# Kernel tuning notes

Hardware: AMD Instinct MI355X
Metric: run time of the kernel (lower is better)

Reference implementation:

```python
import jax, jax.numpy as jnp
import numpy as np

B, S, I, H, O = 64, 2048, 256, 512, 10

def setup_inputs() -> dict:
    key = jax.random.key(0)
    ks = jax.random.split(key, 16)
    s_in = 1.0 / np.sqrt(I)
    s_h = 1.0 / np.sqrt(H)
    return {
        "x": jax.random.normal(ks[0], (B, S, I), dtype=jnp.float32),
        "Wz": jax.random.normal(ks[1], (H, I), dtype=jnp.float32) * s_in,
        "bz": jax.random.normal(ks[2], (H,), dtype=jnp.float32) * s_in,
        "Uz": jax.random.normal(ks[3], (H, H), dtype=jnp.float32) * s_h,
        "cz": jax.random.normal(ks[4], (H,), dtype=jnp.float32) * s_h,
        "Wr": jax.random.normal(ks[5], (H, I), dtype=jnp.float32) * s_in,
        "br": jax.random.normal(ks[6], (H,), dtype=jnp.float32) * s_in,
        "Ur": jax.random.normal(ks[7], (H, H), dtype=jnp.float32) * s_h,
        "cr": jax.random.normal(ks[8], (H,), dtype=jnp.float32) * s_h,
        "Wh": jax.random.normal(ks[9], (H, I), dtype=jnp.float32) * s_in,
        "bh": jax.random.normal(ks[10], (H,), dtype=jnp.float32) * s_in,
        "Uh": jax.random.normal(ks[11], (H, H), dtype=jnp.float32) * s_h,
        "ch": jax.random.normal(ks[12], (H,), dtype=jnp.float32) * s_h,
        "Wf": jax.random.normal(ks[13], (O, H), dtype=jnp.float32) * s_h,
        "bf": jax.random.normal(ks[14], (O,), dtype=jnp.float32) * s_h,
    }


def reference(x, Wz, bz, Uz, cz, Wr, br, Ur, cr, Wh, bh, Uh, ch, Wf, bf):
    b, s, _ = x.shape
    h_dim = Uz.shape[0]
    # Precompute input-gate projections for all timesteps in 3 big GEMMs: [B,S,H]
    xz = jnp.einsum('bsi,hi->bsh', x, Wz) + bz
    xr = jnp.einsum('bsi,hi->bsh', x, Wr) + br
    xh = jnp.einsum('bsi,hi->bsh', x, Wh) + bh
    # scan over time (transpose to time-major [S,B,H])
    xs = (jnp.swapaxes(xz, 0, 1), jnp.swapaxes(xr, 0, 1), jnp.swapaxes(xh, 0, 1))

    def step(h, ins):
        xz_t, xr_t, xh_t = ins
        z = jax.nn.sigmoid(xz_t + h @ Uz.T + cz)
        r = jax.nn.sigmoid(xr_t + h @ Ur.T + cr)
        h_tilde = jnp.tanh(xh_t + (r * h) @ Uh.T + ch)
        h_new = (1.0 - z) * h + z * h_tilde
        return h_new, None

    h0 = jnp.zeros((b, h_dim), dtype=x.dtype)
    h_T, _ = jax.lax.scan(step, h0, xs)
    return h_T @ Wf.T + bf
```

## Files before the change

kernel.cpp:

```cpp
#include <hip/hip_runtime.h>
#include <stdint.h>


#define S_LEN  2048
#define BATCH  64
#define IDIM   256
#define HDIM   512
#define ODIM   10
#define GATES3 1536

typedef __attribute__((ext_vector_type(8))) short bf16x8;
typedef __attribute__((ext_vector_type(4))) float f32x4;

__device__ __forceinline__ unsigned short f2bf(float x) {
    unsigned int u = __float_as_uint(x);
    u += 0x7fffu + ((u >> 16) & 1u);
    return (unsigned short)(u >> 16);
}
__device__ __forceinline__ float bf2f(unsigned short h) {
    return __uint_as_float(((unsigned int)h) << 16);
}

__device__ __forceinline__ unsigned long long g_load64(const void* p) {
    return __hip_atomic_load((const unsigned long long*)p, __ATOMIC_RELAXED, __HIP_MEMORY_SCOPE_AGENT);
}
__device__ __forceinline__ void g_store32(void* p, unsigned int v) {
    __hip_atomic_store((unsigned int*)p, v, __ATOMIC_RELAXED, __HIP_MEMORY_SCOPE_AGENT);
}

__global__ __launch_bounds__(256)
void proj_mfma(const float* __restrict__ x,
               const float* __restrict__ Wz, const float* __restrict__ Wr, const float* __restrict__ Wh,
               const float* __restrict__ bz, const float* __restrict__ cz,
               const float* __restrict__ br, const float* __restrict__ cr,
               const float* __restrict__ bh, const float* __restrict__ ch,
               unsigned short* __restrict__ xp2)
{
    __shared__ unsigned short As[8 * 128 * 8];
    __shared__ unsigned short Bs[8 * 128 * 8];
    const int tid  = threadIdx.x;
    const int wave = tid >> 6;
    const int lane = tid & 63;
    const int quad = lane >> 4;
    const int l16  = lane & 15;
    const int nt_ = blockIdx.x;
    const int mt_ = blockIdx.y;

    const int srow  = tid >> 1;
    const int shalf = tid & 1;
    const int mg = mt_ * 128 + srow;
    const float* axrow = x + ((size_t)(mg & 63) * S_LEN + (mg >> 6)) * IDIM + shalf * 32;
    const int ng = nt_ * 128 + srow;
    const int gt = ng >> 9, hl = ng & 511;
    const float* bxrow = (gt == 0 ? Wz : gt == 1 ? Wr : Wh) + (size_t)hl * IDIM + shalf * 32;

    f32x4 acc[2][8];
#pragma unroll
    for (int mi = 0; mi < 2; ++mi)
#pragma unroll
        for (int nj = 0; nj < 8; ++nj) {
            f32x4 z = {0.f, 0.f, 0.f, 0.f};
            acc[mi][nj] = z;
        }

    for (int kp = 0; kp < IDIM; kp += 64) {
#pragma unroll
        for (int c = 0; c < 4; ++c) {
            unsigned short ta[8], tb[8];
#pragma unroll
            for (int e = 0; e < 8; ++e) {
                ta[e] = f2bf(axrow[kp + c * 8 + e]);
                tb[e] = f2bf(bxrow[kp + c * 8 + e]);
            }
            const int kcq = shalf * 4 + c;
            *(bf16x8*)(As + (kcq * 128 + srow) * 8) = *(bf16x8*)ta;
            *(bf16x8*)(Bs + (kcq * 128 + srow) * 8) = *(bf16x8*)tb;
        }
        __syncthreads();
#pragma unroll
        for (int kc = 0; kc < 2; ++kc) {
            bf16x8 af[2], bfr[8];
#pragma unroll
            for (int mi = 0; mi < 2; ++mi)
                af[mi] = *(const bf16x8*)(As + ((kc * 4 + quad) * 128 + wave * 32 + mi * 16 + l16) * 8);
#pragma unroll
            for (int nj = 0; nj < 8; ++nj)
                bfr[nj] = *(const bf16x8*)(Bs + ((kc * 4 + quad) * 128 + nj * 16 + l16) * 8);
#pragma unroll
            for (int mi = 0; mi < 2; ++mi)
#pragma unroll
                for (int nj = 0; nj < 8; ++nj)
                    acc[mi][nj] = __builtin_amdgcn_mfma_f32_16x16x32_bf16(af[mi], bfr[nj], acc[mi][nj], 0, 0, 0);
        }
        __syncthreads();
    }

    const int s_ = mt_ * 2 + (wave >> 1);
#pragma unroll
    for (int nj = 0; nj < 8; ++nj) {
        const int n  = nt_ * 128 + nj * 16 + l16;
        const int g2 = n >> 9, h2 = n & 511;
        const float bias = (g2 == 0 ? bz[h2] + cz[h2]
                          : g2 == 1 ? br[h2] + cr[h2]
                                    : bh[h2] + ch[h2]);
#pragma unroll
        for (int mi = 0; mi < 2; ++mi) {
            const int gg = (wave & 1) * 2 + mi;
            unsigned short pk[4];
#pragma unroll
            for (int r = 0; r < 4; ++r) pk[r] = f2bf(acc[mi][nj][r] + bias);
            *(unsigned long long*)(xp2 + (((size_t)gg * S_LEN + s_) * GATES3 + n) * 16 + quad * 4) =
                *(unsigned long long*)pk;
        }
    }
}

__device__ __forceinline__ void stage_frag(const unsigned short* __restrict__ gsrc,
                                           unsigned short* __restrict__ lds, int tid)
{
    unsigned long long v[8];
    const unsigned short* p = gsrc + tid * 32;
#pragma unroll
    for (int i = 0; i < 8; ++i) v[i] = g_load64(p + i * 4);
    unsigned long long* q = (unsigned long long*)(lds + tid * 32);
#pragma unroll
    for (int i = 0; i < 8; ++i) q[i] = v[i];
}

__device__ __forceinline__ void group_barrier(unsigned int* __restrict__ flags, int g, int j,
                                              unsigned int epoch, int tid, int lane)
{
    __syncthreads();
    if (tid == 0)
        __hip_atomic_store(&flags[(g * 16 + j) * 16], epoch,
                           __ATOMIC_RELAXED, __HIP_MEMORY_SCOPE_AGENT);
    if (lane < 16) {
        const unsigned int* f = &flags[(g * 16 + lane) * 16];
        while (__hip_atomic_load(f, __ATOMIC_RELAXED, __HIP_MEMORY_SCOPE_AGENT) < epoch)
            __builtin_amdgcn_s_sleep(2);
    }
}

__global__ __launch_bounds__(256)
void gru_recur(const float* __restrict__ Uz, const float* __restrict__ Ur,
               const float* __restrict__ Uh,
               const unsigned short* __restrict__ xp2,
               unsigned short* __restrict__ hg,
               unsigned short* __restrict__ rhg,
               float* __restrict__ hgf,
               unsigned int* __restrict__ flags,
               const float* __restrict__ Wf, const float* __restrict__ bfv,
               float* __restrict__ out)
{
    __shared__ unsigned short ldsA[8192];
    __shared__ unsigned short ldsB[8192];
    __shared__ float hlds[16][33];
    const int tid  = threadIdx.x;
    const int wave = tid >> 6;
    const int lane = tid & 63;
    const int quad = lane >> 4;
    const int l16  = lane & 15;
    const int g  = blockIdx.x & 3;
    const int j  = blockIdx.x >> 2;
    const int b0 = g * 16;
    const int i0 = j * 32;
    const int nt = wave & 1;
    const bool isZ = (wave < 2);

    for (int i = tid; i < 16 * 33; i += 256) (&hlds[0][0])[i] = 0.f;

    const int wrow = i0 + nt * 16 + l16;
    const int kofs = quad * 8;
    bf16x8 wp1[16], wp2[16];
    const float* U1 = isZ ? Uz : Ur;
#pragma unroll
    for (int kb = 0; kb < 16; ++kb) {
        const float* s1 = U1 + (size_t)wrow * HDIM + kb * 32 + kofs;
        const float* s2 = Uh + (size_t)wrow * HDIM + kb * 32 + kofs;
        bf16x8 w1, w2;
#pragma unroll
        for (int e = 0; e < 8; ++e) {
            w1[e] = (short)f2bf(s1[e]);
            w2[e] = (short)f2bf(s2[e]);
        }
        wp1[kb] = w1; wp2[kb] = w2;
    }

    const int iloc = nt * 16 + l16;
    const int icol = i0 + iloc;
    const int pidx = (icol >> 5) * 512 + ((icol >> 3) & 3) * 128 + (icol & 7);
    unsigned short* hgG  = hg  + g * 8192;
    unsigned short* rhgG = rhg + g * 8192;
    const unsigned short* xpg = xp2 + (size_t)g * S_LEN * GATES3 * 16;
    const int gofs1 = isZ ? 0 : HDIM;

    float zfrag[4];
    float hm[4] = {0.f, 0.f, 0.f, 0.f};

    unsigned long long xg_cur = *(const unsigned long long*)
        (xpg + ((size_t)0 * GATES3 + gofs1 + icol) * 16 + quad * 4);
    unsigned long long xh_cur = *(const unsigned long long*)
        (xpg + ((size_t)0 * GATES3 + 2 * HDIM + icol) * 16 + quad * 4);

    __syncthreads();

    for (int t = 0; t < S_LEN; ++t) {
        stage_frag(hgG, ldsA, tid);
        __syncthreads();

        f32x4 c1 = {0.f, 0.f, 0.f, 0.f};
#pragma unroll
        for (int kb = 0; kb < 16; ++kb) {
            const bf16x8 a = *(const bf16x8*)(ldsA + kb * 512 + quad * 128 + l16 * 8);
            c1 = __builtin_amdgcn_mfma_f32_16x16x32_bf16(a, wp1[kb], c1, 0, 0, 0);
        }
        union { unsigned long long q; unsigned short s[4]; } xq;
        xq.q = xg_cur;
        if (isZ) {
#pragma unroll
            for (int r = 0; r < 4; ++r) {
                const float pre = c1[r] + bf2f(xq.s[r]);
                zfrag[r] = 1.f / (1.f + __expf(-pre));
            }
        } else {
#pragma unroll
            for (int r = 0; r < 4; ++r) {
                const float pre = c1[r] + bf2f(xq.s[r]);
                const float v = 1.f / (1.f + __expf(-pre));
                const float rh = v * hlds[quad * 4 + r][iloc];
                unsigned int my = f2bf(rh);
                unsigned int other = (unsigned int)__shfl_xor((int)my, 1, 64);
                if ((lane & 1) == 0)
                    g_store32(rhgG + pidx + (quad * 4 + r) * 8, my | (other << 16));
            }
        }
        group_barrier(flags, g, j, 2u * (unsigned)t + 1u, tid, lane);

        stage_frag(rhgG, ldsB, tid);
        __syncthreads();

        if (isZ) {
            f32x4 c2 = {0.f, 0.f, 0.f, 0.f};
#pragma unroll
            for (int kb = 0; kb < 16; ++kb) {
                const bf16x8 a = *(const bf16x8*)(ldsB + kb * 512 + quad * 128 + l16 * 8);
                c2 = __builtin_amdgcn_mfma_f32_16x16x32_bf16(a, wp2[kb], c2, 0, 0, 0);
            }
            union { unsigned long long q; unsigned short s[4]; } xh;
            xh.q = xh_cur;
            float hn[4];
#pragma unroll
            for (int r = 0; r < 4; ++r) {
                const float pre = c2[r] + bf2f(xh.s[r]);
                const float ht = tanhf(pre);
                hn[r] = hm[r] + zfrag[r] * (ht - hm[r]);
                hm[r] = hn[r];
            }
#pragma unroll
            for (int r = 0; r < 4; ++r) {
                unsigned int my = f2bf(hn[r]);
                unsigned int other = (unsigned int)__shfl_xor((int)my, 1, 64);
                if ((lane & 1) == 0)
                    g_store32(hgG + pidx + (quad * 4 + r) * 8, my | (other << 16));
            }
#pragma unroll
            for (int r = 0; r < 4; ++r) {
                hlds[quad * 4 + r][iloc] = hn[r];
                if (t == S_LEN - 1)
                    g_store32(hgf + (size_t)(b0 + quad * 4 + r) * HDIM + icol,
                              __float_as_uint(hn[r]));
            }
        }
        const int tn = (t + 1 < S_LEN) ? t + 1 : t;
        xg_cur = *(const unsigned long long*)
            (xpg + ((size_t)tn * GATES3 + gofs1 + icol) * 16 + quad * 4);
        xh_cur = *(const unsigned long long*)
            (xpg + ((size_t)tn * GATES3 + 2 * HDIM + icol) * 16 + quad * 4);

        group_barrier(flags, g, j, 2u * (unsigned)t + 2u, tid, lane);
    }

    if (j == 0 && tid < 16 * ODIM) {
        const int b = b0 + tid / ODIM;
        const int o = tid % ODIM;
        float acc = bfv[o];
        for (int k = 0; k < HDIM; k += 2) {
            union { unsigned long long q; float f[2]; } w;
            w.q = g_load64(hgf + (size_t)b * HDIM + k);
            acc += w.f[0] * Wf[o * HDIM + k] + w.f[1] * Wf[o * HDIM + k + 1];
        }
        out[b * ODIM + o] = acc;
    }
}

extern "C" void kernel_launch(void* const* d_in, const int* in_sizes, int n_in,
                              void* d_out, int out_size, void* d_ws, size_t ws_size,
                              hipStream_t stream)
{
    const float* x  = (const float*)d_in[0];
    const float* Wz = (const float*)d_in[1];
    const float* bz = (const float*)d_in[2];
    const float* Uz = (const float*)d_in[3];
    const float* cz = (const float*)d_in[4];
    const float* Wr = (const float*)d_in[5];
    const float* br = (const float*)d_in[6];
    const float* Ur = (const float*)d_in[7];
    const float* cr = (const float*)d_in[8];
    const float* Wh = (const float*)d_in[9];
    const float* bh = (const float*)d_in[10];
    const float* Uh = (const float*)d_in[11];
    const float* ch = (const float*)d_in[12];
    const float* Wf = (const float*)d_in[13];
    const float* bf = (const float*)d_in[14];
    float* out = (float*)d_out;

    char* ws = (char*)d_ws;
    const size_t XPB = (size_t)S_LEN * BATCH * GATES3 * sizeof(unsigned short);
    unsigned short* xp2 = (unsigned short*)ws;
    unsigned short* hg  = (unsigned short*)(ws + XPB);
    unsigned short* rhg = (unsigned short*)(ws + XPB + 65536);
    float*          hgf = (float*)(ws + XPB + 131072);
    unsigned int*   flg = (unsigned int*)(ws + XPB + 262144);

    hipMemsetAsync(ws + XPB, 0, 262144 + 4096, stream);

    proj_mfma<<<dim3(12, 1024), 256, 0, stream>>>(
        x, Wz, Wr, Wh, bz, cz, br, cr, bh, ch, xp2);

    gru_recur<<<dim3(64), dim3(256), 0, stream>>>(
        Uz, Ur, Uh, xp2, hg, rhg, hgf, flg, Wf, bf, out);
}
```

Baseline: 10.93 ms.

## Replace flag barriers with sentinel-polled 4-slot ring buffers for h exchange

Removes the per-step flag-based group barriers and instead has consumers poll the data itself. Hidden-state and r*h buffers become 4-deep rings pre-filled with a 0x7F sentinel, and writers re-poison an older slot after each step. The r-gate path now reads h from the staged LDS copy instead of a separate float tile, stores are widened to 64-bit, and the MFMA chains are split into two accumulators for more ILP. The aim is to cut cross-block synchronization latency per timestep. In exchange it relies on the sentinel bit pattern never occurring as real bf16 data and on the ring depth being safe against fast producers.

Result: slower. 13.58 ms (+24.2%).

```diff
diff --git a/kernel.cpp b/kernel.cpp
--- a/kernel.cpp
+++ b/kernel.cpp
@@ -9,6 +9,9 @@
 #define ODIM   10
 #define GATES3 1536
 
+#define SENT32 0x7F7F7F7Fu
+#define SENT64 0x7F7F7F7F7F7F7F7FULL
+
 typedef __attribute__((ext_vector_type(8))) short bf16x8;
 typedef __attribute__((ext_vector_type(4))) float f32x4;
 
@@ -26,6 +29,9 @@
 }
 __device__ __forceinline__ void g_store32(void* p, unsigned int v) {
     __hip_atomic_store((unsigned int*)p, v, __ATOMIC_RELAXED, __HIP_MEMORY_SCOPE_AGENT);
+}
+__device__ __forceinline__ void g_store64(void* p, unsigned long long v) {
+    __hip_atomic_store((unsigned long long*)p, v, __ATOMIC_RELAXED, __HIP_MEMORY_SCOPE_AGENT);
 }
 
 __global__ __launch_bounds__(256)
@@ -115,29 +121,30 @@
     }
 }
 
-__device__ __forceinline__ void stage_frag(const unsigned short* __restrict__ gsrc,
+__device__ __forceinline__ void stage_poll(const unsigned short* __restrict__ gsrc,
                                            unsigned short* __restrict__ lds, int tid)
 {
     unsigned long long v[8];
-    const unsigned short* p = gsrc + tid * 32;
-#pragma unroll
-    for (int i = 0; i < 8; ++i) v[i] = g_load64(p + i * 4);
-    unsigned long long* q = (unsigned long long*)(lds + tid * 32);
-#pragma unroll
-    for (int i = 0; i < 8; ++i) q[i] = v[i];
-}
-
-__device__ __forceinline__ void group_barrier(unsigned int* __restrict__ flags, int g, int j,
-                                              unsigned int epoch, int tid, int lane)
-{
-    __syncthreads();
-    if (tid == 0)
-        __hip_atomic_store(&flags[(g * 16 + j) * 16], epoch,
-                           __ATOMIC_RELAXED, __HIP_MEMORY_SCOPE_AGENT);
-    if (lane < 16) {
-        const unsigned int* f = &flags[(g * 16 + lane) * 16];
-        while (__hip_atomic_load(f, __ATOMIC_RELAXED, __HIP_MEMORY_SCOPE_AGENT) < epoch)
-            __builtin_amdgcn_s_sleep(2);
+#pragma unroll
+    for (int i = 0; i < 8; ++i)
+        v[i] = g_load64(gsrc + (i >> 1) * 2048 + tid * 8 + (i & 1) * 4);
+    while (true) {
+        unsigned pend = 0;
+#pragma unroll
+        for (int i = 0; i < 8; ++i)
+            if (((unsigned)v[i]) == SENT32 || ((unsigned)(v[i] >> 32)) == SENT32)
+                pend |= 1u << i;
+        if (!pend) break;
+#pragma unroll
+        for (int i = 0; i < 8; ++i)
+            if (pend & (1u << i))
+                v[i] = g_load64(gsrc + (i >> 1) * 2048 + tid * 8 + (i & 1) * 4);
+    }
+#pragma unroll
+    for (int sgm = 0; sgm < 4; ++sgm) {
+        unsigned long long* q = (unsigned long long*)(lds + sgm * 2048 + tid * 8);
+        q[0] = v[2 * sgm];
+        q[1] = v[2 * sgm + 1];
     }
 }
 
@@ -148,13 +155,11 @@
                unsigned short* __restrict__ hg,
                unsigned short* __restrict__ rhg,
                float* __restrict__ hgf,
-               unsigned int* __restrict__ flags,
                const float* __restrict__ Wf, const float* __restrict__ bfv,
                float* __restrict__ out)
 {
     __shared__ unsigned short ldsA[8192];
     __shared__ unsigned short ldsB[8192];
-    __shared__ float hlds[16][33];
     const int tid  = threadIdx.x;
     const int wave = tid >> 6;
     const int lane = tid & 63;
@@ -167,8 +172,6 @@
     const int nt = wave & 1;
     const bool isZ = (wave < 2);
 
-    for (int i = tid; i < 16 * 33; i += 256) (&hlds[0][0])[i] = 0.f;
-
     const int wrow = i0 + nt * 16 + l16;
     const int kofs = quad * 8;
     bf16x8 wp1[16], wp2[16];
@@ -188,9 +191,9 @@
 
     const int iloc = nt * 16 + l16;
     const int icol = i0 + iloc;
-    const int pidx = (icol >> 5) * 512 + ((icol >> 3) & 3) * 128 + (icol & 7);
-    unsigned short* hgG  = hg  + g * 8192;
-    unsigned short* rhgG = rhg + g * 8192;
+    const int pfull = (icol >> 5) * 512 + ((icol >> 3) & 3) * 128 + (icol & 7);
+    const int qbase = (icol >> 5) * 512 + ((icol >> 3) & 3) * 128 + (icol & 4);
+    const bool qlane = ((l16 & 3) == 0);
     const unsigned short* xpg = xp2 + (size_t)g * S_LEN * GATES3 * 16;
     const int gofs1 = isZ ? 0 : HDIM;
 
@@ -202,82 +205,108 @@
     unsigned long long xh_cur = *(const unsigned long long*)
         (xpg + ((size_t)0 * GATES3 + 2 * HDIM + icol) * 16 + quad * 4);
 
-    __syncthreads();
-
     for (int t = 0; t < S_LEN; ++t) {
-        stage_frag(hgG, ldsA, tid);
+        const unsigned short* hsrc = hg + ((((t + 3) & 3) * 4 + g) * 8192);
+        stage_poll(hsrc, ldsA, tid);
         __syncthreads();
 
-        f32x4 c1 = {0.f, 0.f, 0.f, 0.f};
-#pragma unroll
-        for (int kb = 0; kb < 16; ++kb) {
-            const bf16x8 a = *(const bf16x8*)(ldsA + kb * 512 + quad * 128 + l16 * 8);
-            c1 = __builtin_amdgcn_mfma_f32_16x16x32_bf16(a, wp1[kb], c1, 0, 0, 0);
+        f32x4 ca = {0.f, 0.f, 0.f, 0.f}, cb = {0.f, 0.f, 0.f, 0.f};
+#pragma unroll
+        for (int kb = 0; kb < 16; kb += 2) {
+            const bf16x8 a0 = *(const bf16x8*)(ldsA + kb * 512 + quad * 128 + l16 * 8);
+            const bf16x8 a1 = *(const bf16x8*)(ldsA + (kb + 1) * 512 + quad * 128 + l16 * 8);
+            ca = __builtin_amdgcn_mfma_f32_16x16x32_bf16(a0, wp1[kb], ca, 0, 0, 0);
+            cb = __builtin_amdgcn_mfma_f32_16x16x32_bf16(a1, wp1[kb + 1], cb, 0, 0, 0);
         }
         union { unsigned long long q; unsigned short s[4]; } xq;
         xq.q = xg_cur;
+
         if (isZ) {
 #pragma unroll
             for (int r = 0; r < 4; ++r) {
-                const float pre = c1[r] + bf2f(xq.s[r]);
+                const float pre = ca[r] + cb[r] + bf2f(xq.s[r]);
                 zfrag[r] = 1.f / (1.f + __expf(-pre));
             }
         } else {
-#pragma unroll
-            for (int r = 0; r < 4; ++r) {
-                const float pre = c1[r] + bf2f(xq.s[r]);
+            float rhv[4];
+#pragma unroll
+            for (int r = 0; r < 4; ++r) {
+                const float pre = ca[r] + cb[r] + bf2f(xq.s[r]);
                 const float v = 1.f / (1.f + __expf(-pre));
-                const float rh = v * hlds[quad * 4 + r][iloc];
-                unsigned int my = f2bf(rh);
-                unsigned int other = (unsigned int)__shfl_xor((int)my, 1, 64);
-                if ((lane & 1) == 0)
-                    g_store32(rhgG + pidx + (quad * 4 + r) * 8, my | (other << 16));
-            }
-        }
-        group_barrier(flags, g, j, 2u * (unsigned)t + 1u, tid, lane);
-
-        stage_frag(rhgG, ldsB, tid);
+                rhv[r] = v * bf2f(ldsA[pfull + (quad * 4 + r) * 8]);
+            }
+            __builtin_amdgcn_s_waitcnt(0x0F70);
+            unsigned short* ds = rhg + (((t & 3) * 4 + g) * 8192) + qbase;
+            unsigned short* ss = rhg + ((((t + 2) & 3) * 4 + g) * 8192) + qbase;
+#pragma unroll
+            for (int r = 0; r < 4; ++r) {
+                unsigned my = f2bf(rhv[r]);
+                unsigned ot = (unsigned)__shfl_xor((int)my, 1, 64);
+                unsigned d  = my | (ot << 16);
+                unsigned d2 = (unsigned)__shfl_xor((int)d, 2, 64);
+                if (qlane)
+                    g_store64(ds + (quad * 4 + r) * 8,
+                              (unsigned long long)d | ((unsigned long long)d2 << 32));
+            }
+#pragma unroll
+            for (int r = 0; r < 4; ++r)
+                if (qlane) g_store64(ss + (quad * 4 + r) * 8, SENT64);
+            const int tn1 = (t + 1 < S_LEN) ? t + 1 : t;
+            xg_cur = *(const unsigned long long*)
+                (xpg + ((size_t)tn1 * GATES3 + gofs1 + icol) * 16 + quad * 4);
+        }
+
+        const unsigned short* rsrc = rhg + (((t & 3) * 4 + g) * 8192);
+        stage_poll(rsrc, ldsB, tid);
         __syncthreads();
 
         if (isZ) {
-            f32x4 c2 = {0.f, 0.f, 0.f, 0.f};
-#pragma unroll
-            for (int kb = 0; kb < 16; ++kb) {
-                const bf16x8 a = *(const bf16x8*)(ldsB + kb * 512 + quad * 128 + l16 * 8);
-                c2 = __builtin_amdgcn_mfma_f32_16x16x32_bf16(a, wp2[kb], c2, 0, 0, 0);
+            f32x4 c2a = {0.f, 0.f, 0.f, 0.f}, c2b = {0.f, 0.f, 0.f, 0.f};
+#pragma unroll
+            for (int kb = 0; kb < 16; kb += 2) {
+                const bf16x8 a0 = *(const bf16x8*)(ldsB + kb * 512 + quad * 128 + l16 * 8);
+                const bf16x8 a1 = *(const bf16x8*)(ldsB + (kb + 1) * 512 + quad * 128 + l16 * 8);
+                c2a = __builtin_amdgcn_mfma_f32_16x16x32_bf16(a0, wp2[kb], c2a, 0, 0, 0);
+                c2b = __builtin_amdgcn_mfma_f32_16x16x32_bf16(a1, wp2[kb + 1], c2b, 0, 0, 0);
             }
             union { unsigned long long q; unsigned short s[4]; } xh;
             xh.q = xh_cur;
             float hn[4];
 #pragma unroll
             for (int r = 0; r < 4; ++r) {
-                const float pre = c2[r] + bf2f(xh.s[r]);
+                const float pre = c2a[r] + c2b[r] + bf2f(xh.s[r]);
                 const float ht = tanhf(pre);
                 hn[r] = hm[r] + zfrag[r] * (ht - hm[r]);
                 hm[r] = hn[r];
             }
-#pragma unroll
-            for (int r = 0; r < 4; ++r) {
-                unsigned int my = f2bf(hn[r]);
-                unsigned int other = (unsigned int)__shfl_xor((int)my, 1, 64);
-                if ((lane & 1) == 0)
-                    g_store32(hgG + pidx + (quad * 4 + r) * 8, my | (other << 16));
-            }
-#pragma unroll
-            for (int r = 0; r < 4; ++r) {
-                hlds[quad * 4 + r][iloc] = hn[r];
-                if (t == S_LEN - 1)
+            __builtin_amdgcn_s_waitcnt(0x0F70);
+            unsigned short* ds = hg + (((t & 3) * 4 + g) * 8192) + qbase;
+            unsigned short* ss = hg + ((((t + 2) & 3) * 4 + g) * 8192) + qbase;
+#pragma unroll
+            for (int r = 0; r < 4; ++r) {
+                unsigned my = f2bf(hn[r]);
+                unsigned ot = (unsigned)__shfl_xor((int)my, 1, 64);
+                unsigned d  = my | (ot << 16);
+                unsigned d2 = (unsigned)__shfl_xor((int)d, 2, 64);
+                if (qlane)
+                    g_store64(ds + (quad * 4 + r) * 8,
+                              (unsigned long long)d | ((unsigned long long)d2 << 32));
+            }
+#pragma unroll
+            for (int r = 0; r < 4; ++r)
+                if (qlane) g_store64(ss + (quad * 4 + r) * 8, SENT64);
+            if (t == S_LEN - 1) {
+#pragma unroll
+                for (int r = 0; r < 4; ++r)
                     g_store32(hgf + (size_t)(b0 + quad * 4 + r) * HDIM + icol,
                               __float_as_uint(hn[r]));
             }
-        }
-        const int tn = (t + 1 < S_LEN) ? t + 1 : t;
-        xg_cur = *(const unsigned long long*)
-            (xpg + ((size_t)tn * GATES3 + gofs1 + icol) * 16 + quad * 4);
-        xh_cur = *(const unsigned long long*)
-            (xpg + ((size_t)tn * GATES3 + 2 * HDIM + icol) * 16 + quad * 4);
-
-        group_barrier(flags, g, j, 2u * (unsigned)t + 2u, tid, lane);
+            const int tn1 = (t + 1 < S_LEN) ? t + 1 : t;
+            xg_cur = *(const unsigned long long*)
+                (xpg + ((size_t)tn1 * GATES3 + gofs1 + icol) * 16 + quad * 4);
+            xh_cur = *(const unsigned long long*)
+                (xpg + ((size_t)tn1 * GATES3 + 2 * HDIM + icol) * 16 + quad * 4);
+        }
     }
 
     if (j == 0 && tid < 16 * ODIM) {
@@ -285,8 +314,10 @@
         const int o = tid % ODIM;
         float acc = bfv[o];
         for (int k = 0; k < HDIM; k += 2) {
-            union { unsigned long long q; float f[2]; } w;
+            union { unsigned long long q; float f[2]; unsigned u[2]; } w;
             w.q = g_load64(hgf + (size_t)b * HDIM + k);
+            while (w.u[0] == SENT32 || w.u[1] == SENT32)
+                w.q = g_load64(hgf + (size_t)b * HDIM + k);
             acc += w.f[0] * Wf[o * HDIM + k] + w.f[1] * Wf[o * HDIM + k + 1];
         }
         out[b * ODIM + o] = acc;
@@ -318,15 +349,16 @@
     const size_t XPB = (size_t)S_LEN * BATCH * GATES3 * sizeof(unsigned short);
     unsigned short* xp2 = (unsigned short*)ws;
     unsigned short* hg  = (unsigned short*)(ws + XPB);
-    unsigned short* rhg = (unsigned short*)(ws + XPB + 65536);
-    float*          hgf = (float*)(ws + XPB + 131072);
-    unsigned int*   flg = (unsigned int*)(ws + XPB + 262144);
-
-    hipMemsetAsync(ws + XPB, 0, 262144 + 4096, stream);
+    unsigned short* rhg = (unsigned short*)(ws + XPB + 262144);
+    float*          hgf = (float*)(ws + XPB + 524288);
+
+    hipMemsetAsync(ws + XPB, 0x7F, 196608, stream);
+    hipMemsetAsync(ws + XPB + 196608, 0x00, 65536, stream);
+    hipMemsetAsync(ws + XPB + 262144, 0x7F, 262144 + 131072, stream);
 
     proj_mfma<<<dim3(12, 1024), 256, 0, stream>>>(
         x, Wz, Wr, Wh, bz, cz, br, cr, bh, ch, xp2);
 
     gru_recur<<<dim3(64), dim3(256), 0, stream>>>(
-        Uz, Ur, Uh, xp2, hg, rhg, hgf, flg, Wf, bf, out);
-}
+        Uz, Ur, Uh, xp2, hg, rhg, hgf, Wf, bf, out);
+}
```
